# Kernel optimization log

Hardware: AMD Instinct MI355X
Metric: run time of the kernel (lower is better)

Reference implementation:

```python
import jax, jax.numpy as jnp
import numpy as np

B, L, D, H, DH, DEPTH, VOCAB = 8, 512, 256, 8, 64, 16, 5
INNER = 4 * D  # GLU feedforward inner dim = 1024
EPS = 1e-5

def _ln(x, g, b):
    mu = jnp.mean(x, -1, keepdims=True)
    var = jnp.mean(jnp.square(x - mu), -1, keepdims=True)
    return (x - mu) * jax.lax.rsqrt(var + EPS) * g + b

def setup_inputs() -> dict:
    key = jax.random.key(0)
    ks = jax.random.split(key, 24)
    s = 0.02
    seq = jax.random.randint(ks[0], (B, L), 0, VOCAB)
    lengths = jax.random.randint(ks[1], (B,), L // 2, L + 1)
    mask = jnp.arange(L)[None, :] < lengths[:, None]  # [B, L] bool padding mask
    f32 = jnp.float32
    return {
        "seq": seq,
        "mask": mask,
        "emb": jax.random.normal(ks[2], (VOCAB, D), f32) * s,
        "png": jnp.ones((D,), f32), "pnb": jnp.zeros((D,), f32),
        "ln1g": jnp.ones((DEPTH, D), f32), "ln1b": jnp.zeros((DEPTH, D), f32),
        "Wq": jax.random.normal(ks[3], (DEPTH, D, H * DH), f32) * s,
        "Wk": jax.random.normal(ks[4], (DEPTH, D, H * DH), f32) * s,
        "Wv": jax.random.normal(ks[5], (DEPTH, D, H * DH), f32) * s,
        "Wo": jax.random.normal(ks[6], (DEPTH, H * DH, D), f32) * s,
        "ln2g": jnp.ones((DEPTH, D), f32), "ln2b": jnp.zeros((DEPTH, D), f32),
        "W1": jax.random.normal(ks[7], (DEPTH, D, 2 * INNER), f32) * s,
        "b1": jnp.zeros((DEPTH, 2 * INNER), f32),
        "W2": jax.random.normal(ks[8], (DEPTH, INNER, D), f32) * s,
        "b2": jnp.zeros((DEPTH, D), f32),
        "fng": jnp.ones((D,), f32), "fnb": jnp.zeros((D,), f32),
        "Wout": jax.random.normal(ks[9], (D, 2), f32) * s,
        "bout": jnp.zeros((2,), f32),
    }

def _alibi_bias(n):
    # heads=8 is a power of two: slopes = 2^{-1}..2^{-8}
    slopes = 2.0 ** (-(jnp.arange(1, H + 1, dtype=jnp.float32)) * (8.0 / H))
    pos = jnp.arange(n, dtype=jnp.float32)
    rel = -jnp.abs(pos[None, :] - pos[:, None])  # [n, n]
    return slopes[:, None, None] * rel  # [H, n, n]

def _forward(seq, mask, emb, png, pnb, ln1g, ln1b, Wq, Wk, Wv, Wo,
             ln2g, ln2b, W1, b1, W2, b2, fng, fnb, Wout, bout):
    x = emb[seq]                      # [B, L, D]
    x = _ln(x, png, pnb)              # post_emb_norm
    bias = _alibi_bias(L)             # [H, L, L]
    kv_mask = mask[:, None, None, :]  # [B, 1, 1, L]
    scale = DH ** -0.5

    def layer(x, p):
        (g1, c1, wq, wk, wv, wo, g2, c2, w1, bb1, w2, bb2) = p
        h = _ln(x, g1, c1)
        q = (h @ wq).reshape(B, L, H, DH).transpose(0, 2, 1, 3)  # bhld
        k = (h @ wk).reshape(B, L, H, DH).transpose(0, 2, 1, 3)
        v = (h @ wv).reshape(B, L, H, DH).transpose(0, 2, 1, 3)
        scores = jnp.einsum('bhid,bhjd->bhij', q, k) * scale + bias
        scores = jnp.where(kv_mask, scores, jnp.float32(-1e9))
        a = jax.nn.softmax(scores, axis=-1)
        o = jnp.einsum('bhij,bhjd->bhid', a, v)
        o = o.transpose(0, 2, 1, 3).reshape(B, L, H * DH) @ wo
        x = x + o
        h2 = _ln(x, g2, c2)
        u = h2 @ w1 + bb1
        val, gate = jnp.split(u, 2, axis=-1)  # GLU: x * gelu(gate)
        x = x + (val * jax.nn.gelu(gate, approximate=False)) @ w2 + bb2
        return x, None

    x, _ = jax.lax.scan(layer, x, (ln1g, ln1b, Wq, Wk, Wv, Wo, ln2g, ln2b, W1, b1, W2, b2))
    x = _ln(x, fng, fnb)              # final encoder norm
    return x @ Wout + bout            # [B, L, 2]

def reference(seq, mask, emb, png, pnb, ln1g, ln1b, Wq, Wk, Wv, Wo,
              ln2g, ln2b, W1, b1, W2, b2, fng, fnb, Wout, bout):
    return _forward(seq, mask, emb, png, pnb, ln1g, ln1b, Wq, Wk, Wv, Wo,
                    ln2g, ln2b, W1, b1, W2, b2, fng, fnb, Wout, bout)
```

## Files before the change

### kernel.cpp

```cpp
#include <hip/hip_runtime.h>
#include <cstdint>
#include <cstddef>

#define BB 8
#define LL 512
#define DD 256
#define HH 8
#define DHD 64
#define NLAYER 16
#define HDH 512
#define IN2 2048
#define IN1 1024

typedef __attribute__((ext_vector_type(8))) short short8;
typedef __attribute__((ext_vector_type(4))) float floatx4;
typedef __attribute__((ext_vector_type(4))) unsigned short ushort4v;
typedef unsigned short u16;

__device__ __forceinline__ floatx4 mfma16(short8 a, short8 b, floatx4 c) {
  return __builtin_amdgcn_mfma_f32_16x16x32_bf16(a, b, c, 0, 0, 0);
}

__device__ __forceinline__ u16 f2b(float f) {
  union { float f; unsigned u; } x; x.f = f;
  unsigned u = x.u + 0x7fffu + ((x.u >> 16) & 1u);
  return (u16)(u >> 16);
}
__device__ __forceinline__ float b2f(u16 s) {
  union { unsigned u; float f; } x; x.u = ((unsigned)s) << 16;
  return x.f;
}

__device__ __forceinline__ float wave_sum(float s) {
#pragma unroll
  for (int off = 32; off; off >>= 1) s += __shfl_xor(s, off);
  return s;
}

__device__ __forceinline__ void gload_lds16(const u16* g, u16* l) {
  __builtin_amdgcn_global_load_lds((__attribute__((address_space(1))) void*)g,
                                   (__attribute__((address_space(3))) void*)l,
                                   16, 0, 0);
}

template <int NSLOTS, int NTHREADS = 256>
__device__ __forceinline__ void stage_tile(const u16* __restrict__ g, int rowstride,
                                           u16* lds, int tid) {
  int wave = tid >> 6, lane = tid & 63;
#pragma unroll
  for (int j = 0; j < NSLOTS / NTHREADS; ++j) {
    int sbase = j * NTHREADS + wave * 64;
    int slot = sbase + lane;
    int row = slot >> 3;
    int kg = (slot & 7) ^ (row & 7);
    gload_lds16(g + (size_t)row * rowstride + kg * 8, lds + sbase * 8);
  }
}

__device__ __forceinline__ short8 ld_frag(const u16* T, int row, int kg) {
  return *(const short8*)&T[(row << 6) + (((kg ^ row) & 7) << 3)];
}

__device__ __forceinline__ short8 ld_frag128(const u16* T, int row, int kg) {
  int pg = (kg & 8) | ((kg ^ row) & 7);
  return *(const short8*)&T[(row << 7) + (pg << 3)];
}

__device__ __forceinline__ float4 ln_math(const float* __restrict__ x,
                                          const float* __restrict__ g,
                                          const float* __restrict__ b, int t) {
  float4 v = *(const float4*)(x + t * 4);
  float s = wave_sum(v.x + v.y + v.z + v.w);
  float mu = s * (1.0f / DD);
  float dx = v.x - mu, dy = v.y - mu, dz = v.z - mu, dw = v.w - mu;
  float ss = wave_sum(dx * dx + dy * dy + dz * dz + dw * dw);
  float r = rsqrtf(ss * (1.0f / DD) + 1e-5f);
  float4 gg = *(const float4*)(g + t * 4);
  float4 bb = *(const float4*)(b + t * 4);
  float4 o;
  o.x = dx * r * gg.x + bb.x;
  o.y = dy * r * gg.y + bb.y;
  o.z = dz * r * gg.z + bb.z;
  o.w = dw * r * gg.w + bb.w;
  return o;
}

__global__ __launch_bounds__(256) void embed_ln_kernel(
    const int* __restrict__ seq, const float* __restrict__ emb,
    const float* __restrict__ png, const float* __restrict__ pnb,
    const float* __restrict__ g1, const float* __restrict__ b1,
    float* __restrict__ X, u16* __restrict__ H) {
  int row = blockIdx.x * 4 + (threadIdx.x >> 6), t = threadIdx.x & 63;
  int tok = seq[row];
  float4 o = ln_math(emb + (size_t)tok * DD, png, pnb, t);
  *(float4*)(X + (size_t)row * DD + t * 4) = o;
  float s = wave_sum(o.x + o.y + o.z + o.w);
  float mu = s * (1.0f / DD);
  float dx = o.x - mu, dy = o.y - mu, dz = o.z - mu, dw = o.w - mu;
  float ss = wave_sum(dx * dx + dy * dy + dz * dz + dw * dw);
  float r = rsqrtf(ss * (1.0f / DD) + 1e-5f);
  float4 gg = *(const float4*)(g1 + t * 4);
  float4 bb = *(const float4*)(b1 + t * 4);
  ushort4v o4;
  o4[0] = f2b(dx * r * gg.x + bb.x);
  o4[1] = f2b(dy * r * gg.y + bb.y);
  o4[2] = f2b(dz * r * gg.z + bb.z);
  o4[3] = f2b(dw * r * gg.w + bb.w);
  *(ushort4v*)(H + (size_t)row * DD + t * 4) = o4;
}

#define WBUF_LAYER 1310720
__global__ __launch_bounds__(256) void prep_weights_kernel(
    const float* __restrict__ Wq, const float* __restrict__ Wk,
    const float* __restrict__ Wv, const float* __restrict__ Wo,
    const float* __restrict__ W1, const float* __restrict__ W2,
    u16* __restrict__ wbuf_all) {
  __shared__ float tile[32][33];
  int l = blockIdx.x / 1280;
  int bx = blockIdx.x % 1280;
  int tid = threadIdx.x;
  const float* wq = Wq + (size_t)l * DD * HDH;
  const float* wk = Wk + (size_t)l * DD * HDH;
  const float* wv = Wv + (size_t)l * DD * HDH;
  const float* wo = Wo + (size_t)l * HDH * DD;
  const float* w1 = W1 + (size_t)l * DD * IN2;
  const float* w2 = W2 + (size_t)l * IN1 * DD;
  u16* wbuf = wbuf_all + (size_t)l * WBUF_LAYER;

  const float* src; int srcld; u16* dst; int dstld; int dn0, k0, scol0;
  int packW1 = 0;
  if (bx < 384) {
    int t = bx; dn0 = (t % 48) * 32; k0 = (t / 48) * 32;
    scol0 = dn0 & 511;
    src = (dn0 < 512) ? wq : ((dn0 < 1024) ? wk : wv);
    srcld = 512; dst = wbuf; dstld = 256;
  } else if (bx < 512) {
    int t = bx - 384; dn0 = (t % 8) * 32; k0 = (t / 8) * 32; scol0 = dn0;
    src = wo; srcld = 256; dst = wbuf + 393216; dstld = 512;
  } else if (bx < 1024) {
    int t = bx - 512; dn0 = (t % 64) * 32; k0 = (t / 64) * 32; scol0 = dn0;
    src = w1; srcld = 2048; dst = wbuf + 524288; dstld = 256; packW1 = 1;
  } else {
    int t = bx - 1024; dn0 = (t % 8) * 32; k0 = (t / 8) * 32; scol0 = dn0;
    src = w2; srcld = 256; dst = wbuf + 1048576; dstld = 1024;
  }
  int r = tid >> 3, c4 = (tid & 7) * 4;
  float4 v = *(const float4*)&src[(size_t)(k0 + r) * srcld + scol0 + c4];
  tile[r][c4 + 0] = v.x; tile[r][c4 + 1] = v.y;
  tile[r][c4 + 2] = v.z; tile[r][c4 + 3] = v.w;
  __syncthreads();
  int n = tid >> 3, kk = (tid & 7) * 4;
  int drow = dn0 + n;
  if (packW1) {
    if (drow < 1024) drow = ((drow >> 4) << 5) | (drow & 15);
    else { int nn = drow - 1024; drow = (((nn >> 4) << 5) + 16) | (nn & 15); }
  }
  ushort4v o4;
  o4[0] = f2b(tile[kk + 0][n]); o4[1] = f2b(tile[kk + 1][n]);
  o4[2] = f2b(tile[kk + 2][n]); o4[3] = f2b(tile[kk + 3][n]);
  *(ushort4v*)&dst[(size_t)drow * dstld + k0 + kk] = o4;
}

__global__ __launch_bounds__(256) void gemm_qkv(
    const u16* __restrict__ A, const u16* __restrict__ BT,
    u16* __restrict__ qk, u16* __restrict__ vT) {
  __shared__ __align__(16) u16 As[2][128 * 64];
  __shared__ __align__(16) u16 Bs[2][96 * 64];
  int tid = threadIdx.x;
  int wave = tid >> 6, lane = tid & 63;
  int lm = lane & 15, quad = lane >> 4;
  int wr = wave >> 1, wc = wave & 1;
  int n0 = blockIdx.x * 96, m0 = blockIdx.y * 128;
  const u16* Ab = A + (size_t)m0 * DD;
  const u16* Bb = BT + (size_t)n0 * DD;

  floatx4 acc[4][3];
#pragma unroll
  for (int mf = 0; mf < 4; ++mf)
#pragma unroll
    for (int nf = 0; nf < 3; ++nf)
#pragma unroll
      for (int r = 0; r < 4; ++r) acc[mf][nf][r] = 0.0f;

  stage_tile<1024>(Ab, DD, As[0], tid);
  stage_tile<768>(Bb, DD, Bs[0], tid);
  __syncthreads();
#pragma unroll
  for (int it = 0; it < 4; ++it) {
    if (it < 3) {
      stage_tile<1024>(Ab + (it + 1) * 64, DD, As[(it + 1) & 1], tid);
      stage_tile<768>(Bb + (it + 1) * 64, DD, Bs[(it + 1) & 1], tid);
    }
    const u16* Ac = As[it & 1];
    const u16* Bc = Bs[it & 1];
#pragma unroll
    for (int kc = 0; kc < 2; ++kc) {
      short8 af[4], bf[3];
#pragma unroll
      for (int mf = 0; mf < 4; ++mf)
        af[mf] = ld_frag(Ac, wr * 64 + mf * 16 + lm, kc * 4 + quad);
#pragma unroll
      for (int nf = 0; nf < 3; ++nf)
        bf[nf] = ld_frag(Bc, wc * 48 + nf * 16 + lm, kc * 4 + quad);
#pragma unroll
      for (int mf = 0; mf < 4; ++mf)
#pragma unroll
        for (int nf = 0; nf < 3; ++nf)
          acc[mf][nf] = mfma16(af[mf], bf[nf], acc[mf][nf]);
    }
    if (it < 3) __syncthreads();
  }
#pragma unroll
  for (int mf = 0; mf < 4; ++mf)
#pragma unroll
    for (int nf = 0; nf < 3; ++nf) {
      int colf = n0 + wc * 48 + nf * 16;
      if (colf < 1024) {
#pragma unroll
        for (int r = 0; r < 4; ++r) {
          int row = m0 + wr * 64 + mf * 16 + quad * 4 + r;
          qk[(size_t)row * 1024 + colf + lm] = f2b(acc[mf][nf][r]);
        }
      } else {
        int token0 = m0 + wr * 64 + mf * 16 + quad * 4;
        int hd = colf + lm - 1024;
        int b = token0 >> 9, key = token0 & 511;
        ushort4v p4;
#pragma unroll
        for (int r = 0; r < 4; ++r) p4[r] = f2b(acc[mf][nf][r]);
        *(ushort4v*)&vT[((size_t)(b * 8 + (hd >> 6)) * 64 + (hd & 63)) * 512 + key] = p4;
      }
    }
}

__global__ __launch_bounds__(256) void gemm_ffn1(
    const u16* __restrict__ A, const u16* __restrict__ BTp,
    const float* __restrict__ b1, u16* __restrict__ G) {
  __shared__ __align__(16) u16 As[2][128 * 64];
  __shared__ __align__(16) u16 Bs[2][128 * 64];
  int tid = threadIdx.x;
  int wave = tid >> 6, lane = tid & 63;
  int lm = lane & 15, quad = lane >> 4;
  int wr = wave >> 1, wc = wave & 1;
  int n0 = blockIdx.x * 128, m0 = blockIdx.y * 128;
  const u16* Ab = A + (size_t)m0 * DD;
  const u16* Bb = BTp + (size_t)n0 * DD;

  floatx4 acc[4][4];
#pragma unroll
  for (int mf = 0; mf < 4; ++mf)
#pragma unroll
    for (int nf = 0; nf < 4; ++nf)
#pragma unroll
      for (int r = 0; r < 4; ++r) acc[mf][nf][r] = 0.0f;

  stage_tile<1024>(Ab, DD, As[0], tid);
  stage_tile<1024>(Bb, DD, Bs[0], tid);
  __syncthreads();
#pragma unroll
  for (int it = 0; it < 4; ++it) {
    if (it < 3) {
      stage_tile<1024>(Ab + (it + 1) * 64, DD, As[(it + 1) & 1], tid);
      stage_tile<1024>(Bb + (it + 1) * 64, DD, Bs[(it + 1) & 1], tid);
    }
    const u16* Ac = As[it & 1];
    const u16* Bc = Bs[it & 1];
#pragma unroll
    for (int kc = 0; kc < 2; ++kc) {
      short8 af[4], bf[4];
#pragma unroll
      for (int mf = 0; mf < 4; ++mf)
        af[mf] = ld_frag(Ac, wr * 64 + mf * 16 + lm, kc * 4 + quad);
#pragma unroll
      for (int nf = 0; nf < 4; ++nf)
        bf[nf] = ld_frag(Bc, wc * 64 + nf * 16 + lm, kc * 4 + quad);
#pragma unroll
      for (int mf = 0; mf < 4; ++mf)
#pragma unroll
        for (int nf = 0; nf < 4; ++nf)
          acc[mf][nf] = mfma16(af[mf], bf[nf], acc[mf][nf]);
    }
    if (it < 3) __syncthreads();
  }
  int p0 = (n0 + wc * 64) >> 5;
#pragma unroll
  for (int j = 0; j < 2; ++j) {
    int gcol = (p0 + j) * 16 + lm;
    float bv = b1[gcol], bg = b1[1024 + gcol];
#pragma unroll
    for (int mf = 0; mf < 4; ++mf)
#pragma unroll
      for (int r = 0; r < 4; ++r) {
        int row = m0 + wr * 64 + mf * 16 + quad * 4 + r;
        float val = acc[mf][2 * j][r] + bv;
        float gate = acc[mf][2 * j + 1][r] + bg;
        float ge = 0.5f * gate * (1.0f + erff(gate * 0.70710678118654752440f));
        G[(size_t)row * IN1 + gcol] = f2b(val * ge);
      }
  }
}

__global__ __launch_bounds__(512) void gemm_row_ln(
    const u16* __restrict__ A, int lda, const u16* __restrict__ BT, int K,
    const float* __restrict__ bias, float* __restrict__ X,
    const float* __restrict__ lng, const float* __restrict__ lnb,
    u16* __restrict__ Hout,
    const float* __restrict__ Wout, const float* __restrict__ bout,
    float* __restrict__ outp) {
  __shared__ __align__(16) u16 As[2][16 * 128];
  __shared__ __align__(16) u16 Bs[2][256 * 128];
  int tid = threadIdx.x;
  int wave = tid >> 6, lane = tid & 63;
  int lm = lane & 15, quad = lane >> 4;
  int m0 = blockIdx.x * 16;

  floatx4 acc[2];
#pragma unroll
  for (int nf = 0; nf < 2; ++nf)
#pragma unroll
    for (int r = 0; r < 4; ++r) acc[nf][r] = 0.0f;

  const u16* Ab = A + (size_t)m0 * lda;

  auto stageA = [&](int k0, u16* dst) {
    if (wave < 4) {
      int sbase = wave * 64;
      int slot = sbase + lane;
      int row = slot >> 4, pg = slot & 15;
      int kg = (pg & 8) | ((pg ^ row) & 7);
      gload_lds16(Ab + (size_t)row * lda + k0 + kg * 8, dst + sbase * 8);
    }
  };
  auto stageB = [&](int k0, u16* dst) {
#pragma unroll
    for (int j = 0; j < 8; ++j) {
      int sbase = j * 512 + wave * 64;
      int slot = sbase + lane;
      int row = slot >> 4, pg = slot & 15;
      int kg = (pg & 8) | ((pg ^ row) & 7);
      gload_lds16(BT + (size_t)row * K + k0 + kg * 8, dst + sbase * 8);
    }
  };

  stageA(0, As[0]);
  stageB(0, Bs[0]);
  __syncthreads();
  int iters = K >> 7;
  for (int it = 0; it < iters; ++it) {
    if (it + 1 < iters) {
      stageA((it + 1) * 128, As[(it + 1) & 1]);
      stageB((it + 1) * 128, Bs[(it + 1) & 1]);
    }
    const u16* Ac = As[it & 1];
    const u16* Bc = Bs[it & 1];
#pragma unroll
    for (int kc = 0; kc < 4; ++kc) {
      short8 af = ld_frag128(Ac, lm, kc * 4 + quad);
#pragma unroll
      for (int nf = 0; nf < 2; ++nf) {
        short8 bf = ld_frag128(Bc, wave * 32 + nf * 16 + lm, kc * 4 + quad);
        acc[nf] = mfma16(af, bf, acc[nf]);
      }
    }
    if (it + 1 < iters) __syncthreads();
  }
  __syncthreads();
  float* xs = (float*)Bs[0];
#pragma unroll
  for (int nf = 0; nf < 2; ++nf) {
    int col = wave * 32 + nf * 16 + lm;
    float bv = bias ? bias[col] : 0.0f;
#pragma unroll
    for (int r = 0; r < 4; ++r) {
      int row = quad * 4 + r;
      float v = acc[nf][r] + bv + X[(size_t)(m0 + row) * DD + col];
      X[(size_t)(m0 + row) * DD + col] = v;
      xs[row * DD + col] = v;
    }
  }
  __syncthreads();
  float4 gg = *(const float4*)(lng + lane * 4);
  float4 bb = *(const float4*)(lnb + lane * 4);
#pragma unroll
  for (int rr = 0; rr < 2; ++rr) {
    int row = wave * 2 + rr;
    float4 v = *(const float4*)&xs[row * DD + lane * 4];
    float s = wave_sum(v.x + v.y + v.z + v.w);
    float mu = s * (1.0f / DD);
    float dx = v.x - mu, dy = v.y - mu, dz = v.z - mu, dw = v.w - mu;
    float ss = wave_sum(dx * dx + dy * dy + dz * dz + dw * dw);
    float rc = rsqrtf(ss * (1.0f / DD) + 1e-5f);
    float o0 = dx * rc * gg.x + bb.x;
    float o1 = dy * rc * gg.y + bb.y;
    float o2 = dz * rc * gg.z + bb.z;
    float o3 = dw * rc * gg.w + bb.w;
    ushort4v o4;
    o4[0] = f2b(o0); o4[1] = f2b(o1); o4[2] = f2b(o2); o4[3] = f2b(o3);
    *(ushort4v*)(Hout + (size_t)(m0 + row) * DD + lane * 4) = o4;
    if (Wout) {
      int d0 = lane * 4;
      float s0 = o0 * Wout[d0 * 2] + o1 * Wout[(d0 + 1) * 2] +
                 o2 * Wout[(d0 + 2) * 2] + o3 * Wout[(d0 + 3) * 2];
      float s1 = o0 * Wout[d0 * 2 + 1] + o1 * Wout[(d0 + 1) * 2 + 1] +
                 o2 * Wout[(d0 + 2) * 2 + 1] + o3 * Wout[(d0 + 3) * 2 + 1];
      s0 = wave_sum(s0);
      s1 = wave_sum(s1);
      if (lane == 0) {
        outp[(size_t)(m0 + row) * 2 + 0] = s0 + bout[0];
        outp[(size_t)(m0 + row) * 2 + 1] = s1 + bout[1];
      }
    }
  }
}

__global__ __launch_bounds__(512) void attn_mfma_kernel(
    const u16* __restrict__ qk, const u16* __restrict__ vT,
    const int* __restrict__ mask_raw, u16* __restrict__ O) {
  __shared__ __align__(16) u16 Ks[2][64 * 64];
  __shared__ __align__(16) u16 Vs[2][64 * 64];
  __shared__ __align__(16) u16 Ps[8][16][72];
  __shared__ __align__(16) float madd[64];

  const int tid = threadIdx.x, wave = tid >> 6, lane = tid & 63;
  const int lm = lane & 15, quad = lane >> 4;
  const int qb = blockIdx.x, h = blockIdx.y, b = blockIdx.z;
  const float slope = exp2f(-(float)(h + 1));

  int w0 = mask_raw[0];
  int mmode = (w0 == 1) ? 0 : ((w0 == 0x3f800000) ? 2 : 1);
  const int krow_base = b * LL;

  int ntv = 8;
#pragma unroll
  for (int t = 7; t >= 0; --t) {
    bool tv;
    int gi = krow_base + t * 64;
    if (mmode == 0) tv = mask_raw[gi] != 0;
    else if (mmode == 1) tv = ((const signed char*)mask_raw)[gi] != 0;
    else tv = ((const float*)mask_raw)[gi] != 0.0f;
    if (!tv) ntv = t;
  }

  const int q0 = qb * 128 + wave * 16;
  const int qg = b * LL + q0;
  const float qpos = (float)(q0 + lm);

  const u16* qp = qk + (size_t)(qg + lm) * 1024 + h * 64 + quad * 8;
  short8 qf0 = *(const short8*)qp;
  short8 qf1 = *(const short8*)(qp + 32);

  floatx4 oc[4];
#pragma unroll
  for (int nf = 0; nf < 4; ++nf)
#pragma unroll
    for (int r = 0; r < 4; ++r) oc[nf][r] = 0.0f;
  float mrow = -1e30f, lrow = 0.0f;

  const u16* kbase_p = qk + (size_t)krow_base * 1024 + 512 + h * 64;
  const u16* vbase = vT + (size_t)(b * 8 + h) * 64 * 512;

  stage_tile<512, 512>(kbase_p, 1024, Ks[0], tid);
  stage_tile<512, 512>(vbase, 512, Vs[0], tid);
  if (tid < 64) {
    int gi = krow_base + (ntv - 1) * 64 + tid;
    bool valid;
    if (mmode == 0) valid = mask_raw[gi] != 0;
    else if (mmode == 1) valid = ((const signed char*)mask_raw)[gi] != 0;
    else valid = ((const float*)mask_raw)[gi] != 0.0f;
    madd[tid] = valid ? 0.0f : -1e9f;
  }
  __syncthreads();

  for (int t = 0; t < ntv; ++t) {
    int k0 = t * 64;
    if (t + 1 < ntv) {
      stage_tile<512, 512>(kbase_p + (size_t)(t + 1) * 64 * 1024, 1024,
                           Ks[(t + 1) & 1], tid);
      stage_tile<512, 512>(vbase + (t + 1) * 64, 512, Vs[(t + 1) & 1], tid);
    }
    const u16* Kc = Ks[t & 1];
    const u16* Vc = Vs[t & 1];
    bool bnd = (t == ntv - 1);

    float sc[4][4];
    float tmax = -3e38f;
#pragma unroll
    for (int nt = 0; nt < 4; ++nt) {
      floatx4 pc;
#pragma unroll
      for (int r = 0; r < 4; ++r) pc[r] = 0.0f;
      short8 kf0 = ld_frag(Kc, nt * 16 + lm, quad);
      short8 kf1 = ld_frag(Kc, nt * 16 + lm, 4 + quad);
      pc = mfma16(kf0, qf0, pc);
      pc = mfma16(kf1, qf1, pc);
      float kbase = (float)(k0 + nt * 16 + quad * 4);
#pragma unroll
      for (int r = 0; r < 4; ++r) {
        float s = pc[r] * 0.125f - slope * fabsf(qpos - (kbase + r));
        sc[nt][r] = s;
      }
      if (bnd) {
        float4 ma = *(const float4*)&madd[nt * 16 + quad * 4];
#pragma unroll
        for (int r = 0; r < 4; ++r) sc[nt][r] += ((const float*)&ma)[r];
      }
#pragma unroll
      for (int r = 0; r < 4; ++r) tmax = fmaxf(tmax, sc[nt][r]);
    }
    tmax = fmaxf(tmax, __shfl_xor(tmax, 16));
    tmax = fmaxf(tmax, __shfl_xor(tmax, 32));
    float nm = fmaxf(mrow, tmax);
    float alpha = __expf(mrow - nm);
    mrow = nm;
    float rsum = 0.0f;
#pragma unroll
    for (int nt = 0; nt < 4; ++nt)
#pragma unroll
      for (int r = 0; r < 4; ++r) {
        float p = __expf(sc[nt][r] - nm);
        sc[nt][r] = p;
        rsum += p;
      }
    rsum += __shfl_xor(rsum, 16);
    rsum += __shfl_xor(rsum, 32);
    lrow = lrow * alpha + rsum;
    float av[4];
#pragma unroll
    for (int r = 0; r < 4; ++r) av[r] = __shfl(alpha, quad * 4 + r);
#pragma unroll
    for (int nf = 0; nf < 4; ++nf)
#pragma unroll
      for (int r = 0; r < 4; ++r) oc[nf][r] *= av[r];
#pragma unroll
    for (int nt = 0; nt < 4; ++nt) {
      ushort4v p4;
#pragma unroll
      for (int r = 0; r < 4; ++r) p4[r] = f2b(sc[nt][r]);
      *(ushort4v*)&Ps[wave][lm][nt * 16 + quad * 4] = p4;
    }
#pragma unroll
    for (int kc = 0; kc < 2; ++kc) {
      short8 af = *(const short8*)&Ps[wave][lm][kc * 32 + quad * 8];
#pragma unroll
      for (int nf = 0; nf < 4; ++nf) {
        short8 bv = ld_frag(Vc, nf * 16 + lm, kc * 4 + quad);
        oc[nf] = mfma16(af, bv, oc[nf]);
      }
    }
    if (t + 1 < ntv) __syncthreads();
  }
  float rl = 1.0f / lrow;
  float rv[4];
#pragma unroll
  for (int r = 0; r < 4; ++r) rv[r] = __shfl(rl, quad * 4 + r);
#pragma unroll
  for (int nf = 0; nf < 4; ++nf)
#pragma unroll
    for (int r = 0; r < 4; ++r) {
      int qq = qg + quad * 4 + r;
      O[(size_t)qq * HDH + h * 64 + nf * 16 + lm] = f2b(oc[nf][r] * rv[r]);
    }
}

extern "C" void kernel_launch(void* const* d_in, const int* in_sizes, int n_in,
                              void* d_out, int out_size, void* d_ws, size_t ws_size,
                              hipStream_t stream) {
  const int* seq = (const int*)d_in[0];
  const int* mask = (const int*)d_in[1];
  const float* emb = (const float*)d_in[2];
  const float* png = (const float*)d_in[3];
  const float* pnb = (const float*)d_in[4];
  const float* ln1g = (const float*)d_in[5];
  const float* ln1b = (const float*)d_in[6];
  const float* Wq = (const float*)d_in[7];
  const float* Wk = (const float*)d_in[8];
  const float* Wv = (const float*)d_in[9];
  const float* Wo = (const float*)d_in[10];
  const float* ln2g = (const float*)d_in[11];
  const float* ln2b = (const float*)d_in[12];
  const float* W1 = (const float*)d_in[13];
  const float* b1 = (const float*)d_in[14];
  const float* W2 = (const float*)d_in[15];
  const float* b2 = (const float*)d_in[16];
  const float* fng = (const float*)d_in[17];
  const float* fnb = (const float*)d_in[18];
  const float* Wout = (const float*)d_in[19];
  const float* bout = (const float*)d_in[20];
  float* out = (float*)d_out;

  uint8_t* wsb = (uint8_t*)d_ws;
  float* x = (float*)(wsb + 0);
  u16* hb = (u16*)(wsb + 4194304);
  u16* wbuf = (u16*)(wsb + 6291456);
  u16* qk = (u16*)(wsb + 48234496);
  u16* vT = (u16*)(wsb + 56623104);
  u16* obuf = (u16*)(wsb + 60817408);
  u16* gbuf = (u16*)(wsb + 65011712);

  const int M = BB * LL;

  prep_weights_kernel<<<16 * 1280, 256, 0, stream>>>(Wq, Wk, Wv, Wo, W1, W2, wbuf);
  embed_ln_kernel<<<M / 4, 256, 0, stream>>>(seq, emb, png, pnb, ln1g, ln1b, x, hb);

  for (int l = 0; l < NLAYER; ++l) {
    u16* wl = wbuf + (size_t)l * WBUF_LAYER;

    gemm_qkv<<<dim3(1536 / 96, M / 128), 256, 0, stream>>>(hb, wl, qk, vT);

    attn_mfma_kernel<<<dim3(LL / 128, HH, BB), 512, 0, stream>>>(qk, vT, mask, obuf);

    gemm_row_ln<<<M / 16, 512, 0, stream>>>(
        obuf, HDH, wl + 393216, HDH, nullptr, x,
        ln2g + l * DD, ln2b + l * DD, hb, nullptr, nullptr, nullptr);

    gemm_ffn1<<<dim3(IN2 / 128, M / 128), 256, 0, stream>>>(
        hb, wl + 524288, b1 + (size_t)l * IN2, gbuf);

    const float* ng = (l < NLAYER - 1) ? (ln1g + (l + 1) * DD) : fng;
    const float* nb = (l < NLAYER - 1) ? (ln1b + (l + 1) * DD) : fnb;
    const float* wo_p = (l == NLAYER - 1) ? Wout : nullptr;
    const float* bo_p = (l == NLAYER - 1) ? bout : nullptr;
    float* out_p = (l == NLAYER - 1) ? out : nullptr;
    gemm_row_ln<<<M / 16, 512, 0, stream>>>(
        gbuf, IN1, wl + 1048576, IN1, b2 + (size_t)l * DD, x, ng, nb, hb,
        wo_p, bo_p, out_p);
  }

  (void)in_sizes; (void)n_in; (void)out_size; (void)ws_size;
}
```

Before: 1.223 ms.

## Fuse all layer stages into one persistent kernel with grid barriers

Replaces the 80 per-layer kernel launches with a single persistent kernel of 256 blocks of 512 threads. Each layer runs QKV, attention, the two row-LN GEMMs and FFN1 as device stages separated by a software atomic grid barrier. Each stage's tiling is remapped to 256 blocks: QKV uses 128x192 tiles, FFN1 loops over two tiles per block with narrower n-fragments, and shared memory is one 136 KB buffer. This removes launch overhead and inter-kernel gaps. In exchange it relies on all 256 blocks being co-resident (deadlock risk otherwise), pays barrier latency, and has less parallelism per stage.

```diff
diff --git a/kernel.cpp b/kernel.cpp
--- a/kernel.cpp
+++ b/kernel.cpp
@@ -11,6 +11,7 @@
 #define HDH 512
 #define IN2 2048
 #define IN1 1024
+#define NBLK 256u
 
 typedef __attribute__((ext_vector_type(8))) short short8;
 typedef __attribute__((ext_vector_type(4))) float floatx4;
@@ -64,6 +65,28 @@
 __device__ __forceinline__ short8 ld_frag128(const u16* T, int row, int kg) {
   int pg = (kg & 8) | ((kg ^ row) & 7);
   return *(const short8*)&T[(row << 7) + (pg << 3)];
+}
+
+__device__ __forceinline__ void grid_barrier(unsigned* cnt, unsigned* gen,
+                                             unsigned p) {
+  __syncthreads();
+  if (threadIdx.x == 0) {
+    __threadfence();
+    if (atomicAdd(cnt, 1u) == NBLK - 1) {
+      atomicExch(cnt, 0u);
+      __threadfence();
+      atomicExch(gen, p);
+    } else {
+      unsigned g;
+      do {
+        g = __hip_atomic_load(gen, __ATOMIC_RELAXED, __HIP_MEMORY_SCOPE_AGENT);
+        if ((int)(g - p) >= 0) break;
+        __builtin_amdgcn_s_sleep(2);
+      } while (true);
+    }
+    __threadfence();
+  }
+  __syncthreads();
 }
 
 __device__ __forceinline__ float4 ln_math(const float* __restrict__ x,
@@ -161,18 +184,18 @@
   *(ushort4v*)&dst[(size_t)drow * dstld + k0 + kk] = o4;
 }
 
-__global__ __launch_bounds__(256) void gemm_qkv(
-    const u16* __restrict__ A, const u16* __restrict__ BT,
-    u16* __restrict__ qk, u16* __restrict__ vT) {
-  __shared__ __align__(16) u16 As[2][128 * 64];
-  __shared__ __align__(16) u16 Bs[2][96 * 64];
-  int tid = threadIdx.x;
+
+__device__ __forceinline__ void stage_qkv(
+    const u16* __restrict__ hb, const u16* __restrict__ wl,
+    u16* __restrict__ qk, u16* __restrict__ vT, u16* smem, int tid, int bx) {
+  u16* AsA[2] = {smem, smem + 8192};
+  u16* BsA[2] = {smem + 16384, smem + 28672};
   int wave = tid >> 6, lane = tid & 63;
   int lm = lane & 15, quad = lane >> 4;
-  int wr = wave >> 1, wc = wave & 1;
-  int n0 = blockIdx.x * 96, m0 = blockIdx.y * 128;
-  const u16* Ab = A + (size_t)m0 * DD;
-  const u16* Bb = BT + (size_t)n0 * DD;
+  int wr = wave >> 2, wc = wave & 3;
+  int m0 = (bx >> 3) * 128, n0 = (bx & 7) * 192;
+  const u16* Ab = hb + (size_t)m0 * DD;
+  const u16* Bb = wl + (size_t)n0 * DD;
 
   floatx4 acc[4][3];
 #pragma unroll
@@ -182,17 +205,17 @@
 #pragma unroll
       for (int r = 0; r < 4; ++r) acc[mf][nf][r] = 0.0f;
 
-  stage_tile<1024>(Ab, DD, As[0], tid);
-  stage_tile<768>(Bb, DD, Bs[0], tid);
+  stage_tile<1024, 512>(Ab, DD, AsA[0], tid);
+  stage_tile<1536, 512>(Bb, DD, BsA[0], tid);
   __syncthreads();
 #pragma unroll
   for (int it = 0; it < 4; ++it) {
     if (it < 3) {
-      stage_tile<1024>(Ab + (it + 1) * 64, DD, As[(it + 1) & 1], tid);
-      stage_tile<768>(Bb + (it + 1) * 64, DD, Bs[(it + 1) & 1], tid);
-    }
-    const u16* Ac = As[it & 1];
-    const u16* Bc = Bs[it & 1];
+      stage_tile<1024, 512>(Ab + (it + 1) * 64, DD, AsA[(it + 1) & 1], tid);
+      stage_tile<1536, 512>(Bb + (it + 1) * 64, DD, BsA[(it + 1) & 1], tid);
+    }
+    const u16* Ac = AsA[it & 1];
+    const u16* Bc = BsA[it & 1];
 #pragma unroll
     for (int kc = 0; kc < 2; ++kc) {
       short8 af[4], bf[3];
@@ -233,86 +256,168 @@
     }
 }
 
-__global__ __launch_bounds__(256) void gemm_ffn1(
-    const u16* __restrict__ A, const u16* __restrict__ BTp,
-    const float* __restrict__ b1, u16* __restrict__ G) {
-  __shared__ __align__(16) u16 As[2][128 * 64];
-  __shared__ __align__(16) u16 Bs[2][128 * 64];
-  int tid = threadIdx.x;
-  int wave = tid >> 6, lane = tid & 63;
-  int lm = lane & 15, quad = lane >> 4;
-  int wr = wave >> 1, wc = wave & 1;
-  int n0 = blockIdx.x * 128, m0 = blockIdx.y * 128;
-  const u16* Ab = A + (size_t)m0 * DD;
-  const u16* Bb = BTp + (size_t)n0 * DD;
-
-  floatx4 acc[4][4];
-#pragma unroll
-  for (int mf = 0; mf < 4; ++mf)
+__device__ __forceinline__ void stage_attn(
+    const u16* __restrict__ qk, const u16* __restrict__ vT,
+    const int* __restrict__ mask_raw, u16* __restrict__ O,
+    u16* smem, int tid, int bx) {
+  u16* Ks2[2] = {smem, smem + 4096};
+  u16* Vs2[2] = {smem + 8192, smem + 12288};
+  u16* Ps = smem + 16384;
+  float* madd = (float*)(smem + 25600);
+
+  const int wave = tid >> 6, lane = tid & 63;
+  const int lm = lane & 15, quad = lane >> 4;
+  const int qb = bx & 3, h = (bx >> 2) & 7, b = bx >> 5;
+  const float slope = exp2f(-(float)(h + 1));
+
+  int w0 = mask_raw[0];
+  int mmode = (w0 == 1) ? 0 : ((w0 == 0x3f800000) ? 2 : 1);
+  const int krow_base = b * LL;
+
+  int ntv = 8;
+#pragma unroll
+  for (int t = 7; t >= 0; --t) {
+    bool tv;
+    int gi = krow_base + t * 64;
+    if (mmode == 0) tv = mask_raw[gi] != 0;
+    else if (mmode == 1) tv = ((const signed char*)mask_raw)[gi] != 0;
+    else tv = ((const float*)mask_raw)[gi] != 0.0f;
+    if (!tv) ntv = t;
+  }
+
+  const int q0 = qb * 128 + wave * 16;
+  const int qg = b * LL + q0;
+  const float qpos = (float)(q0 + lm);
+
+  const u16* qp = qk + (size_t)(qg + lm) * 1024 + h * 64 + quad * 8;
+  short8 qf0 = *(const short8*)qp;
+  short8 qf1 = *(const short8*)(qp + 32);
+
+  floatx4 oc[4];
+#pragma unroll
+  for (int nf = 0; nf < 4; ++nf)
+#pragma unroll
+    for (int r = 0; r < 4; ++r) oc[nf][r] = 0.0f;
+  float mrow = -1e30f, lrow = 0.0f;
+
+  const u16* kbase_p = qk + (size_t)krow_base * 1024 + 512 + h * 64;
+  const u16* vbase = vT + (size_t)(b * 8 + h) * 64 * 512;
+
+  stage_tile<512, 512>(kbase_p, 1024, Ks2[0], tid);
+  stage_tile<512, 512>(vbase, 512, Vs2[0], tid);
+  if (tid < 64) {
+    int gi = krow_base + (ntv - 1) * 64 + tid;
+    bool valid;
+    if (mmode == 0) valid = mask_raw[gi] != 0;
+    else if (mmode == 1) valid = ((const signed char*)mask_raw)[gi] != 0;
+    else valid = ((const float*)mask_raw)[gi] != 0.0f;
+    madd[tid] = valid ? 0.0f : -1e9f;
+  }
+  __syncthreads();
+
+  for (int t = 0; t < ntv; ++t) {
+    int k0 = t * 64;
+    if (t + 1 < ntv) {
+      stage_tile<512, 512>(kbase_p + (size_t)(t + 1) * 64 * 1024, 1024,
+                           Ks2[(t + 1) & 1], tid);
+      stage_tile<512, 512>(vbase + (t + 1) * 64, 512, Vs2[(t + 1) & 1], tid);
+    }
+    const u16* Kc = Ks2[t & 1];
+    const u16* Vc = Vs2[t & 1];
+    bool bnd = (t == ntv - 1);
+
+    float sc[4][4];
+    float tmax = -3e38f;
+#pragma unroll
+    for (int nt = 0; nt < 4; ++nt) {
+      floatx4 pc;
+#pragma unroll
+      for (int r = 0; r < 4; ++r) pc[r] = 0.0f;
+      short8 kf0 = ld_frag(Kc, nt * 16 + lm, quad);
+      short8 kf1 = ld_frag(Kc, nt * 16 + lm, 4 + quad);
+      pc = mfma16(kf0, qf0, pc);
+      pc = mfma16(kf1, qf1, pc);
+      float kbase = (float)(k0 + nt * 16 + quad * 4);
+#pragma unroll
+      for (int r = 0; r < 4; ++r) {
+        float s = pc[r] * 0.125f - slope * fabsf(qpos - (kbase + r));
+        sc[nt][r] = s;
+      }
+      if (bnd) {
+        float4 ma = *(const float4*)&madd[nt * 16 + quad * 4];
+#pragma unroll
+        for (int r = 0; r < 4; ++r) sc[nt][r] += ((const float*)&ma)[r];
+      }
+#pragma unroll
+      for (int r = 0; r < 4; ++r) tmax = fmaxf(tmax, sc[nt][r]);
+    }
+    tmax = fmaxf(tmax, __shfl_xor(tmax, 16));
+    tmax = fmaxf(tmax, __shfl_xor(tmax, 32));
+    float nm = fmaxf(mrow, tmax);
+    float alpha = __expf(mrow - nm);
+    mrow = nm;
+    float rsum = 0.0f;
+#pragma unroll
+    for (int nt = 0; nt < 4; ++nt)
+#pragma unroll
+      for (int r = 0; r < 4; ++r) {
+        float p = __expf(sc[nt][r] - nm);
+        sc[nt][r] = p;
+        rsum += p;
+      }
+    rsum += __shfl_xor(rsum, 16);
+    rsum += __shfl_xor(rsum, 32);
+    lrow = lrow * alpha + rsum;
+    float av[4];
+#pragma unroll
+    for (int r = 0; r < 4; ++r) av[r] = __shfl(alpha, quad * 4 + r);
 #pragma unroll
     for (int nf = 0; nf < 4; ++nf)
 #pragma unroll
-      for (int r = 0; r < 4; ++r) acc[mf][nf][r] = 0.0f;
-
-  stage_tile<1024>(Ab, DD, As[0], tid);
-  stage_tile<1024>(Bb, DD, Bs[0], tid);
-  __syncthreads();
-#pragma unroll
-  for (int it = 0; it < 4; ++it) {
-    if (it < 3) {
-      stage_tile<1024>(Ab + (it + 1) * 64, DD, As[(it + 1) & 1], tid);
-      stage_tile<1024>(Bb + (it + 1) * 64, DD, Bs[(it + 1) & 1], tid);
-    }
-    const u16* Ac = As[it & 1];
-    const u16* Bc = Bs[it & 1];
+      for (int r = 0; r < 4; ++r) oc[nf][r] *= av[r];
+#pragma unroll
+    for (int nt = 0; nt < 4; ++nt) {
+      ushort4v p4;
+#pragma unroll
+      for (int r = 0; r < 4; ++r) p4[r] = f2b(sc[nt][r]);
+      *(ushort4v*)&Ps[(wave * 16 + lm) * 72 + nt * 16 + quad * 4] = p4;
+    }
 #pragma unroll
     for (int kc = 0; kc < 2; ++kc) {
-      short8 af[4], bf[4];
-#pragma unroll
-      for (int mf = 0; mf < 4; ++mf)
-        af[mf] = ld_frag(Ac, wr * 64 + mf * 16 + lm, kc * 4 + quad);
-#pragma unroll
-      for (int nf = 0; nf < 4; ++nf)
-        bf[nf] = ld_frag(Bc, wc * 64 + nf * 16 + lm, kc * 4 + quad);
-#pragma unroll
-      for (int mf = 0; mf < 4; ++mf)
-#pragma unroll
-        for (int nf = 0; nf < 4; ++nf)
-          acc[mf][nf] = mfma16(af[mf], bf[nf], acc[mf][nf]);
-    }
-    if (it < 3) __syncthreads();
-  }
-  int p0 = (n0 + wc * 64) >> 5;
-#pragma unroll
-  for (int j = 0; j < 2; ++j) {
-    int gcol = (p0 + j) * 16 + lm;
-    float bv = b1[gcol], bg = b1[1024 + gcol];
-#pragma unroll
-    for (int mf = 0; mf < 4; ++mf)
-#pragma unroll
-      for (int r = 0; r < 4; ++r) {
-        int row = m0 + wr * 64 + mf * 16 + quad * 4 + r;
-        float val = acc[mf][2 * j][r] + bv;
-        float gate = acc[mf][2 * j + 1][r] + bg;
-        float ge = 0.5f * gate * (1.0f + erff(gate * 0.70710678118654752440f));
-        G[(size_t)row * IN1 + gcol] = f2b(val * ge);
-      }
-  }
-}
-
-__global__ __launch_bounds__(512) void gemm_row_ln(
+      short8 af = *(const short8*)&Ps[(wave * 16 + lm) * 72 + kc * 32 + quad * 8];
+#pragma unroll
+      for (int nf = 0; nf < 4; ++nf) {
+        short8 bv = ld_frag(Vc, nf * 16 + lm, kc * 4 + quad);
+        oc[nf] = mfma16(af, bv, oc[nf]);
+      }
+    }
+    if (t + 1 < ntv) __syncthreads();
+  }
+  float rl = 1.0f / lrow;
+  float rv[4];
+#pragma unroll
+  for (int r = 0; r < 4; ++r) rv[r] = __shfl(rl, quad * 4 + r);
+#pragma unroll
+  for (int nf = 0; nf < 4; ++nf)
+#pragma unroll
+    for (int r = 0; r < 4; ++r) {
+      int qq = qg + quad * 4 + r;
+      O[(size_t)qq * HDH + h * 64 + nf * 16 + lm] = f2b(oc[nf][r] * rv[r]);
+    }
+}
+
+__device__ __forceinline__ void stage_rowln(
     const u16* __restrict__ A, int lda, const u16* __restrict__ BT, int K,
     const float* __restrict__ bias, float* __restrict__ X,
     const float* __restrict__ lng, const float* __restrict__ lnb,
     u16* __restrict__ Hout,
     const float* __restrict__ Wout, const float* __restrict__ bout,
-    float* __restrict__ outp) {
-  __shared__ __align__(16) u16 As[2][16 * 128];
-  __shared__ __align__(16) u16 Bs[2][256 * 128];
-  int tid = threadIdx.x;
+    float* __restrict__ outp, u16* smem, int tid, int bx) {
+  u16* AsB[2] = {smem, smem + 2048};
+  u16* BsB[2] = {smem + 4096, smem + 36864};
   int wave = tid >> 6, lane = tid & 63;
   int lm = lane & 15, quad = lane >> 4;
-  int m0 = blockIdx.x * 16;
+  int m0 = bx * 16;
 
   floatx4 acc[2];
 #pragma unroll
@@ -342,17 +447,17 @@
     }
   };
 
-  stageA(0, As[0]);
-  stageB(0, Bs[0]);
+  stageA(0, AsB[0]);
+  stageB(0, BsB[0]);
   __syncthreads();
   int iters = K >> 7;
   for (int it = 0; it < iters; ++it) {
     if (it + 1 < iters) {
-      stageA((it + 1) * 128, As[(it + 1) & 1]);
-      stageB((it + 1) * 128, Bs[(it + 1) & 1]);
-    }
-    const u16* Ac = As[it & 1];
-    const u16* Bc = Bs[it & 1];
+      stageA((it + 1) * 128, AsB[(it + 1) & 1]);
+      stageB((it + 1) * 128, BsB[(it + 1) & 1]);
+    }
+    const u16* Ac = AsB[it & 1];
+    const u16* Bc = BsB[it & 1];
 #pragma unroll
     for (int kc = 0; kc < 4; ++kc) {
       short8 af = ld_frag128(Ac, lm, kc * 4 + quad);
@@ -365,7 +470,7 @@
     if (it + 1 < iters) __syncthreads();
   }
   __syncthreads();
-  float* xs = (float*)Bs[0];
+  float* xs = (float*)BsB[0];
 #pragma unroll
   for (int nf = 0; nf < 2; ++nf) {
     int col = wave * 32 + nf * 16 + lm;
@@ -413,153 +518,118 @@
   }
 }
 
-__global__ __launch_bounds__(512) void attn_mfma_kernel(
-    const u16* __restrict__ qk, const u16* __restrict__ vT,
-    const int* __restrict__ mask_raw, u16* __restrict__ O) {
-  __shared__ __align__(16) u16 Ks[2][64 * 64];
-  __shared__ __align__(16) u16 Vs[2][64 * 64];
-  __shared__ __align__(16) u16 Ps[8][16][72];
-  __shared__ __align__(16) float madd[64];
-
-  const int tid = threadIdx.x, wave = tid >> 6, lane = tid & 63;
-  const int lm = lane & 15, quad = lane >> 4;
-  const int qb = blockIdx.x, h = blockIdx.y, b = blockIdx.z;
-  const float slope = exp2f(-(float)(h + 1));
-
-  int w0 = mask_raw[0];
-  int mmode = (w0 == 1) ? 0 : ((w0 == 0x3f800000) ? 2 : 1);
-  const int krow_base = b * LL;
-
-  int ntv = 8;
-#pragma unroll
-  for (int t = 7; t >= 0; --t) {
-    bool tv;
-    int gi = krow_base + t * 64;
-    if (mmode == 0) tv = mask_raw[gi] != 0;
-    else if (mmode == 1) tv = ((const signed char*)mask_raw)[gi] != 0;
-    else tv = ((const float*)mask_raw)[gi] != 0.0f;
-    if (!tv) ntv = t;
-  }
-
-  const int q0 = qb * 128 + wave * 16;
-  const int qg = b * LL + q0;
-  const float qpos = (float)(q0 + lm);
-
-  const u16* qp = qk + (size_t)(qg + lm) * 1024 + h * 64 + quad * 8;
-  short8 qf0 = *(const short8*)qp;
-  short8 qf1 = *(const short8*)(qp + 32);
-
-  floatx4 oc[4];
-#pragma unroll
-  for (int nf = 0; nf < 4; ++nf)
-#pragma unroll
-    for (int r = 0; r < 4; ++r) oc[nf][r] = 0.0f;
-  float mrow = -1e30f, lrow = 0.0f;
-
-  const u16* kbase_p = qk + (size_t)krow_base * 1024 + 512 + h * 64;
-  const u16* vbase = vT + (size_t)(b * 8 + h) * 64 * 512;
-
-  stage_tile<512, 512>(kbase_p, 1024, Ks[0], tid);
-  stage_tile<512, 512>(vbase, 512, Vs[0], tid);
-  if (tid < 64) {
-    int gi = krow_base + (ntv - 1) * 64 + tid;
-    bool valid;
-    if (mmode == 0) valid = mask_raw[gi] != 0;
-    else if (mmode == 1) valid = ((const signed char*)mask_raw)[gi] != 0;
-    else valid = ((const float*)mask_raw)[gi] != 0.0f;
-    madd[tid] = valid ? 0.0f : -1e9f;
-  }
-  __syncthreads();
-
-  for (int t = 0; t < ntv; ++t) {
-    int k0 = t * 64;
-    if (t + 1 < ntv) {
-      stage_tile<512, 512>(kbase_p + (size_t)(t + 1) * 64 * 1024, 1024,
-                           Ks[(t + 1) & 1], tid);
-      stage_tile<512, 512>(vbase + (t + 1) * 64, 512, Vs[(t + 1) & 1], tid);
-    }
-    const u16* Kc = Ks[t & 1];
-    const u16* Vc = Vs[t & 1];
-    bool bnd = (t == ntv - 1);
-
-    float sc[4][4];
-    float tmax = -3e38f;
-#pragma unroll
-    for (int nt = 0; nt < 4; ++nt) {
-      floatx4 pc;
-#pragma unroll
-      for (int r = 0; r < 4; ++r) pc[r] = 0.0f;
-      short8 kf0 = ld_frag(Kc, nt * 16 + lm, quad);
-      short8 kf1 = ld_frag(Kc, nt * 16 + lm, 4 + quad);
-      pc = mfma16(kf0, qf0, pc);
-      pc = mfma16(kf1, qf1, pc);
-      float kbase = (float)(k0 + nt * 16 + quad * 4);
+__device__ __forceinline__ void stage_ffn1(
+    const u16* __restrict__ hb, const u16* __restrict__ w1p,
+    const float* __restrict__ b1l, u16* __restrict__ G,
+    u16* smem, int tid, int bx) {
+  u16* AsF[2] = {smem, smem + 8192};
+  u16* BsF[2] = {smem + 16384, smem + 24576};
+  int wave = tid >> 6, lane = tid & 63;
+  int lm = lane & 15, quad = lane >> 4;
+  int wr = wave >> 2, wc = wave & 3;
+
+  for (int t2 = 0; t2 < 2; ++t2) {
+    int tile = bx + t2 * 256;
+    int n0 = (tile & 15) * 128, m0 = (tile >> 4) * 128;
+    const u16* Ab = hb + (size_t)m0 * DD;
+    const u16* Bb = w1p + (size_t)n0 * DD;
+    if (t2) __syncthreads();
+
+    floatx4 acc[4][2];
+#pragma unroll
+    for (int mf = 0; mf < 4; ++mf)
+#pragma unroll
+      for (int nf = 0; nf < 2; ++nf)
+#pragma unroll
+        for (int r = 0; r < 4; ++r) acc[mf][nf][r] = 0.0f;
+
+    stage_tile<1024, 512>(Ab, DD, AsF[0], tid);
+    stage_tile<1024, 512>(Bb, DD, BsF[0], tid);
+    __syncthreads();
+#pragma unroll
+    for (int it = 0; it < 4; ++it) {
+      if (it < 3) {
+        stage_tile<1024, 512>(Ab + (it + 1) * 64, DD, AsF[(it + 1) & 1], tid);
+        stage_tile<1024, 512>(Bb + (it + 1) * 64, DD, BsF[(it + 1) & 1], tid);
+      }
+      const u16* Ac = AsF[it & 1];
+      const u16* Bc = BsF[it & 1];
+#pragma unroll
+      for (int kc = 0; kc < 2; ++kc) {
+        short8 af[4], bf[2];
+#pragma unroll
+        for (int mf = 0; mf < 4; ++mf)
+          af[mf] = ld_frag(Ac, wr * 64 + mf * 16 + lm, kc * 4 + quad);
+#pragma unroll
+        for (int nf = 0; nf < 2; ++nf)
+          bf[nf] = ld_frag(Bc, wc * 32 + nf * 16 + lm, kc * 4 + quad);
+#pragma unroll
+        for (int mf = 0; mf < 4; ++mf)
+#pragma unroll
+          for (int nf = 0; nf < 2; ++nf)
+            acc[mf][nf] = mfma16(af[mf], bf[nf], acc[mf][nf]);
+      }
+      if (it < 3) __syncthreads();
+    }
+    int p0 = (n0 + wc * 32) >> 5;
+    int gcol = p0 * 16 + lm;
+    float bv = b1l[gcol], bg = b1l[1024 + gcol];
+#pragma unroll
+    for (int mf = 0; mf < 4; ++mf)
 #pragma unroll
       for (int r = 0; r < 4; ++r) {
-        float s = pc[r] * 0.125f - slope * fabsf(qpos - (kbase + r));
-        sc[nt][r] = s;
-      }
-      if (bnd) {
-        float4 ma = *(const float4*)&madd[nt * 16 + quad * 4];
-#pragma unroll
-        for (int r = 0; r < 4; ++r) sc[nt][r] += ((const float*)&ma)[r];
-      }
-#pragma unroll
-      for (int r = 0; r < 4; ++r) tmax = fmaxf(tmax, sc[nt][r]);
-    }
-    tmax = fmaxf(tmax, __shfl_xor(tmax, 16));
-    tmax = fmaxf(tmax, __shfl_xor(tmax, 32));
-    float nm = fmaxf(mrow, tmax);
-    float alpha = __expf(mrow - nm);
-    mrow = nm;
-    float rsum = 0.0f;
-#pragma unroll
-    for (int nt = 0; nt < 4; ++nt)
-#pragma unroll
-      for (int r = 0; r < 4; ++r) {
-        float p = __expf(sc[nt][r] - nm);
-        sc[nt][r] = p;
-        rsum += p;
-      }
-    rsum += __shfl_xor(rsum, 16);
-    rsum += __shfl_xor(rsum, 32);
-    lrow = lrow * alpha + rsum;
-    float av[4];
-#pragma unroll
-    for (int r = 0; r < 4; ++r) av[r] = __shfl(alpha, quad * 4 + r);
-#pragma unroll
-    for (int nf = 0; nf < 4; ++nf)
-#pragma unroll
-      for (int r = 0; r < 4; ++r) oc[nf][r] *= av[r];
-#pragma unroll
-    for (int nt = 0; nt < 4; ++nt) {
-      ushort4v p4;
-#pragma unroll
-      for (int r = 0; r < 4; ++r) p4[r] = f2b(sc[nt][r]);
-      *(ushort4v*)&Ps[wave][lm][nt * 16 + quad * 4] = p4;
-    }
-#pragma unroll
-    for (int kc = 0; kc < 2; ++kc) {
-      short8 af = *(const short8*)&Ps[wave][lm][kc * 32 + quad * 8];
-#pragma unroll
-      for (int nf = 0; nf < 4; ++nf) {
-        short8 bv = ld_frag(Vc, nf * 16 + lm, kc * 4 + quad);
-        oc[nf] = mfma16(af, bv, oc[nf]);
-      }
-    }
-    if (t + 1 < ntv) __syncthreads();
-  }
-  float rl = 1.0f / lrow;
-  float rv[4];
-#pragma unroll
-  for (int r = 0; r < 4; ++r) rv[r] = __shfl(rl, quad * 4 + r);
-#pragma unroll
-  for (int nf = 0; nf < 4; ++nf)
-#pragma unroll
-    for (int r = 0; r < 4; ++r) {
-      int qq = qg + quad * 4 + r;
-      O[(size_t)qq * HDH + h * 64 + nf * 16 + lm] = f2b(oc[nf][r] * rv[r]);
-    }
+        int row = m0 + wr * 64 + mf * 16 + quad * 4 + r;
+        float val = acc[mf][0][r] + bv;
+        float gate = acc[mf][1][r] + bg;
+        float ge = 0.5f * gate * (1.0f + erff(gate * 0.70710678118654752440f));
+        G[(size_t)row * IN1 + gcol] = f2b(val * ge);
+      }
+  }
+}
+
+__global__ __launch_bounds__(512, 2) void layers_kernel(
+    const int* __restrict__ mask, const u16* __restrict__ wbuf,
+    u16* __restrict__ qk, u16* __restrict__ vT,
+    u16* __restrict__ obuf, u16* __restrict__ gbuf,
+    u16* __restrict__ hb, float* __restrict__ x,
+    const float* __restrict__ b1, const float* __restrict__ b2,
+    const float* __restrict__ ln2g, const float* __restrict__ ln2b,
+    const float* __restrict__ ln1g, const float* __restrict__ ln1b,
+    const float* __restrict__ fng, const float* __restrict__ fnb,
+    const float* __restrict__ Wout, const float* __restrict__ bout,
+    float* __restrict__ out, unsigned* __restrict__ bar) {
+  __shared__ __align__(16) u16 smem[69632];
+  int tid = threadIdx.x, bx = blockIdx.x;
+  unsigned* cnt = bar;
+  unsigned* gen = bar + 1;
+  unsigned phase = 0;
+
+#pragma unroll 1
+  for (int l = 0; l < NLAYER; ++l) {
+    const u16* wl = wbuf + (size_t)l * WBUF_LAYER;
+
+    stage_qkv(hb, wl, qk, vT, smem, tid, bx);
+    grid_barrier(cnt, gen, ++phase);
+
+    stage_attn(qk, vT, mask, obuf, smem, tid, bx);
+    grid_barrier(cnt, gen, ++phase);
+
+    stage_rowln(obuf, HDH, wl + 393216, HDH, nullptr, x,
+                ln2g + l * DD, ln2b + l * DD, hb,
+                nullptr, nullptr, nullptr, smem, tid, bx);
+    grid_barrier(cnt, gen, ++phase);
+
+    stage_ffn1(hb, wl + 524288, b1 + (size_t)l * IN2, gbuf, smem, tid, bx);
+    grid_barrier(cnt, gen, ++phase);
+
+    const float* ng = (l < NLAYER - 1) ? (ln1g + (l + 1) * DD) : fng;
+    const float* nb = (l < NLAYER - 1) ? (ln1b + (l + 1) * DD) : fnb;
+    stage_rowln(gbuf, IN1, wl + 1048576, IN1, b2 + (size_t)l * DD, x, ng, nb, hb,
+                (l == NLAYER - 1) ? Wout : nullptr,
+                (l == NLAYER - 1) ? bout : nullptr,
+                (l == NLAYER - 1) ? out : nullptr, smem, tid, bx);
+    if (l < NLAYER - 1) grid_barrier(cnt, gen, ++phase);
+  }
 }
 
 extern "C" void kernel_launch(void* const* d_in, const int* in_sizes, int n_in,
@@ -596,35 +666,17 @@
   u16* vT = (u16*)(wsb + 56623104);
   u16* obuf = (u16*)(wsb + 60817408);
   u16* gbuf = (u16*)(wsb + 65011712);
+  unsigned* bar = (unsigned*)(wsb + 73400320);
 
   const int M = BB * LL;
 
+  hipMemsetAsync(bar, 0, 64, stream);
   prep_weights_kernel<<<16 * 1280, 256, 0, stream>>>(Wq, Wk, Wv, Wo, W1, W2, wbuf);
   embed_ln_kernel<<<M / 4, 256, 0, stream>>>(seq, emb, png, pnb, ln1g, ln1b, x, hb);
 
-  for (int l = 0; l < NLAYER; ++l) {
-    u16* wl = wbuf + (size_t)l * WBUF_LAYER;
-
-    gemm_qkv<<<dim3(1536 / 96, M / 128), 256, 0, stream>>>(hb, wl, qk, vT);
-
-    attn_mfma_kernel<<<dim3(LL / 128, HH, BB), 512, 0, stream>>>(qk, vT, mask, obuf);
-
-    gemm_row_ln<<<M / 16, 512, 0, stream>>>(
-        obuf, HDH, wl + 393216, HDH, nullptr, x,
-        ln2g + l * DD, ln2b + l * DD, hb, nullptr, nullptr, nullptr);
-
-    gemm_ffn1<<<dim3(IN2 / 128, M / 128), 256, 0, stream>>>(
-        hb, wl + 524288, b1 + (size_t)l * IN2, gbuf);
-
-    const float* ng = (l < NLAYER - 1) ? (ln1g + (l + 1) * DD) : fng;
-    const float* nb = (l < NLAYER - 1) ? (ln1b + (l + 1) * DD) : fnb;
-    const float* wo_p = (l == NLAYER - 1) ? Wout : nullptr;
-    const float* bo_p = (l == NLAYER - 1) ? bout : nullptr;
-    float* out_p = (l == NLAYER - 1) ? out : nullptr;
-    gemm_row_ln<<<M / 16, 512, 0, stream>>>(
-        gbuf, IN1, wl + 1048576, IN1, b2 + (size_t)l * DD, x, ng, nb, hb,
-        wo_p, bo_p, out_p);
-  }
+  layers_kernel<<<NBLK, 512, 0, stream>>>(
+      mask, wbuf, qk, vT, obuf, gbuf, hb, x, b1, b2, ln2g, ln2b, ln1g, ln1b,
+      fng, fnb, Wout, bout, out, bar);
 
   (void)in_sizes; (void)n_in; (void)out_size; (void)ws_size;
 }
```

Result: slower. 2.893 ms (+136.6%).
